# Kernel optimization log

Measured on AMD Instinct MI355X. Metric: run time of the kernel, lower is better.

Reference implementation:

```python
import jax, jax.numpy as jnp
import numpy as np

N_SITES = 100000
DIM = 128
KSIZE = 7  # 7^3 = 343 offsets
GRID = 160


def _build_sparse_structure(seed=0):
    """Sample N_SITES unique voxels in a GRID^3 volume and build the
    depthwise-conv kernel map: neighbor_idx[i, k] = index of site at
    coords[i] + offset[k], or N_SITES (sentinel -> zero row) if absent."""
    rng = np.random.default_rng(seed)
    lin = rng.choice(GRID ** 3, size=N_SITES, replace=False)
    coords = np.stack(np.unravel_index(lin, (GRID, GRID, GRID)), axis=1).astype(np.int64)  # [N,3]
    lookup = np.full(GRID ** 3, N_SITES, dtype=np.int32)
    lookup[lin] = np.arange(N_SITES, dtype=np.int32)
    r = KSIZE // 2
    offs = np.stack(np.meshgrid(*([np.arange(-r, r + 1)] * 3), indexing="ij"), axis=-1).reshape(-1, 3)  # [343,3]
    K = offs.shape[0]
    neighbor_idx = np.full((N_SITES, K), N_SITES, dtype=np.int32)
    for k in range(K):
        nb = coords + offs[k]
        ok = np.all((nb >= 0) & (nb < GRID), axis=1)
        nb_lin = (nb[ok, 0] * GRID + nb[ok, 1]) * GRID + nb[ok, 2]
        neighbor_idx[ok, k] = lookup[nb_lin]
    return neighbor_idx


def setup_inputs() -> dict:
    key = jax.random.key(0)
    ks = jax.random.split(key, 12)
    neighbor_idx = jnp.asarray(_build_sparse_structure(0))
    d, h = DIM, 4 * DIM
    K = KSIZE ** 3
    return {
        "feats": jax.random.normal(ks[0], (N_SITES, d), jnp.float32),
        "neighbor_idx": neighbor_idx,
        "dw_w": jax.random.normal(ks[1], (K, d), jnp.float32) * 0.05,
        "dw_b": jax.random.normal(ks[2], (d,), jnp.float32) * 0.02,
        "ln_g": 1.0 + 0.1 * jax.random.normal(ks[3], (d,), jnp.float32),
        "ln_b": 0.02 * jax.random.normal(ks[4], (d,), jnp.float32),
        "w1": jax.random.normal(ks[5], (d, h), jnp.float32) * (1.0 / np.sqrt(d)),
        "b1": 0.02 * jax.random.normal(ks[6], (h,), jnp.float32),
        "grn_g": 0.1 * jax.random.normal(ks[7], (1, h), jnp.float32),
        "grn_b": 0.02 * jax.random.normal(ks[8], (1, h), jnp.float32),
        "w2": jax.random.normal(ks[9], (h, d), jnp.float32) * (1.0 / np.sqrt(h)),
        "b2": 0.02 * jax.random.normal(ks[10], (d,), jnp.float32),
    }


def reference(feats, neighbor_idx, dw_w, dw_b, ln_g, ln_b, w1, b1, grn_g, grn_b, w2, b2):
    eps = 1e-6
    n, d = feats.shape
    # --- sparse depthwise conv: gather-multiply-accumulate over kernel offsets ---
    f_pad = jnp.concatenate([feats, jnp.zeros((1, d), feats.dtype)], axis=0)  # sentinel row

    def step(acc, xs):
        idx_k, w_k = xs  # idx_k: [N], w_k: [dim]
        return acc + f_pad[idx_k] * w_k, None

    x, _ = jax.lax.scan(step, jnp.zeros_like(feats), (neighbor_idx.T, dw_w))
    x = x + dw_b
    # --- LayerNorm over channels ---
    mu = jnp.mean(x, axis=-1, keepdims=True)
    var = jnp.var(x, axis=-1, keepdims=True)
    x = (x - mu) / jnp.sqrt(var + eps) * ln_g + ln_b
    # --- pwconv1 -> GELU (exact, matching torch default) ---
    x = jax.nn.gelu(x @ w1 + b1, approximate=False)  # [N, 4*dim]
    # --- GRN: L2 norm over all sites (dim=0), per channel ---
    gx = jnp.sqrt(jnp.sum(x * x, axis=0, keepdims=True))  # [1, 4*dim]
    nx = gx / (jnp.mean(gx, axis=-1, keepdims=True) + eps)
    x = grn_g * (x * nx) + grn_b + x
    # --- pwconv2 + residual (drop_path identity in eval) ---
    x = x @ w2 + b2
    return feats + x
```

## Files before the change

### kernel.cpp

```cpp
#include <hip/hip_runtime.h>

typedef unsigned short u16;
typedef unsigned int u32;
typedef __attribute__((ext_vector_type(8))) short bf16x8;
typedef __attribute__((ext_vector_type(4))) float f32x4;

__device__ __forceinline__ u16 f2bf(float f) {
    u32 u = __float_as_uint(f);
    return (u16)((u + 0x7FFFu + ((u >> 16) & 1u)) >> 16);
}

__device__ __forceinline__ float fast_gelu(float x) {
    const float t = x * x;
    const float y2 = x * __builtin_fmaf(0.0713548214f, t, 1.5957691216057308f);
    const float u = __expf(fminf(y2, 80.f));
    return x * u * __builtin_amdgcn_rcpf(u + 1.f);
}

__device__ __forceinline__ void gload_lds16(const u16* g, u16* l) {
    __builtin_amdgcn_global_load_lds(
        (const __attribute__((address_space(1))) void*)g,
        (__attribute__((address_space(3))) void*)l, 16, 0, 0);
}

__global__ __launch_bounds__(256) void dwln_k(
    const float* __restrict__ feats, const int* __restrict__ nb,
    const float* __restrict__ dw_w, const float* __restrict__ dw_b,
    const float* __restrict__ ln_g, const float* __restrict__ ln_b,
    u16* __restrict__ xln, int nsites)
{
    __shared__ int lists[4][344];
    const int w = threadIdx.x >> 6;
    const int lane = threadIdx.x & 63;
    const int s = blockIdx.x * 4 + w;
    if (s >= nsites) return;
    const int* row = nb + (size_t)s * 343;
    int idx[6];
    #pragma unroll
    for (int j = 0; j < 5; ++j) idx[j] = row[lane + j * 64];
    idx[5] = (lane < 23) ? row[320 + lane] : nsites;
    int c = 0;
    #pragma unroll
    for (int i = 0; i < 6; ++i) c += (idx[i] < nsites) ? 1 : 0;
    int pre = c;
    #pragma unroll
    for (int off = 1; off < 64; off <<= 1) {
        const int v = __shfl_up(pre, off, 64);
        if (lane >= off) pre += v;
    }
    const int cnt = __shfl(pre, 63, 64);
    pre -= c;
    int p = pre;
    #pragma unroll
    for (int i = 0; i < 6; ++i) {
        const int k = (i < 5) ? (lane + i * 64) : (320 + lane);
        if (idx[i] < nsites) lists[w][p++] = idx[i] | (k << 17);
    }
    float x0 = 0.f, x1 = 0.f;
    for (int base = 0; base < cnt; base += 8) {
        float2 f[8], wv[8];
        #pragma unroll
        for (int i = 0; i < 8; ++i) {
            if (base + i < cnt) {
                const int e = lists[w][base + i];
                f[i]  = *(const float2*)(feats + (size_t)(e & 0x1FFFF) * 128 + lane * 2);
                wv[i] = *(const float2*)(dw_w + (size_t)(e >> 17) * 128 + lane * 2);
            } else { f[i] = float2{0.f, 0.f}; wv[i] = float2{0.f, 0.f}; }
        }
        #pragma unroll
        for (int i = 0; i < 8; ++i) {
            x0 += f[i].x * wv[i].x;
            x1 += f[i].y * wv[i].y;
        }
    }
    const float2 bv = *(const float2*)(dw_b + lane * 2);
    const float2 gv = *(const float2*)(ln_g + lane * 2);
    const float2 lbv = *(const float2*)(ln_b + lane * 2);
    float a0 = x0 + bv.x, a1 = x1 + bv.y;
    float sm = a0 + a1, ss = a0 * a0 + a1 * a1;
    #pragma unroll
    for (int off = 32; off > 0; off >>= 1) {
        sm += __shfl_xor(sm, off, 64);
        ss += __shfl_xor(ss, off, 64);
    }
    const float mean = sm * (1.f / 128.f);
    const float var = ss * (1.f / 128.f) - mean * mean;
    const float rstd = rsqrtf(fmaxf(var, 0.f) + 1e-6f);
    const float y0 = (a0 - mean) * rstd * gv.x + lbv.x;
    const float y1 = (a1 - mean) * rstd * gv.y + lbv.y;
    *(u32*)(xln + (size_t)s * 128 + lane * 2) =
        (u32)f2bf(y0) | ((u32)f2bf(y1) << 16);
}

__global__ __launch_bounds__(256) void transpose_w1_k(
    const float* __restrict__ w1, u16* __restrict__ w1t)
{
    const int e = blockIdx.x * 256 + threadIdx.x;
    const int n = e >> 7, k = e & 127;
    w1t[e] = f2bf(w1[k * 512 + n]);
}

__global__ __launch_bounds__(256, 4) void gemm1_k(
    const u16* __restrict__ xln, const u16* __restrict__ w1t,
    const float* __restrict__ b1, u16* __restrict__ h,
    float* __restrict__ gx_sq, int nsites)
{
    __shared__ u16 xb[64 * 128];
    __shared__ float s_red[128];
    const int t = threadIdx.x;
    const int n0 = blockIdx.x * 128;
    const int m0 = blockIdx.y * 64;
    const int lane = t & 63;
    const int w = t >> 6;
    const int wn = w * 32;
    const int l15 = lane & 15, quad = lane >> 4;
    if (t < 128) s_red[t] = 0.f;
    #pragma unroll
    for (int i = 0; i < 4; ++i) {
        const int r = w * 16 + i * 4 + (lane >> 4);
        const int c = (lane & 15) ^ (r & 15);
        gload_lds16(xln + (size_t)(m0 + r) * 128 + c * 8,
                    &xb[(w * 16 + i * 4) * 128]);
    }
    f32x4 acc[2][4];
    #pragma unroll
    for (int i = 0; i < 2; ++i)
        #pragma unroll
        for (int j = 0; j < 4; ++j) acc[i][j] = f32x4{0.f, 0.f, 0.f, 0.f};
    const u16* a_base = w1t + (size_t)(n0 + wn + l15) * 128 + quad * 8;
    bf16x8 aC[2];
    #pragma unroll
    for (int nt = 0; nt < 2; ++nt) aC[nt] = *(const bf16x8*)(a_base + (size_t)nt * 16 * 128);
    asm volatile("s_waitcnt vmcnt(0)" ::: "memory");
    __syncthreads();
    #pragma unroll
    for (int ks = 0; ks < 4; ++ks) {
        bf16x8 aN[2];
        if (ks < 3) {
            #pragma unroll
            for (int nt = 0; nt < 2; ++nt)
                aN[nt] = *(const bf16x8*)(a_base + (size_t)nt * 16 * 128 + (ks + 1) * 32);
        }
        bf16x8 b[4];
        #pragma unroll
        for (int mt = 0; mt < 4; ++mt) {
            const int r = mt * 16 + l15;
            b[mt] = *(const bf16x8*)(&xb[r * 128 + (((ks * 4 + quad) ^ l15) << 3)]);
        }
        #pragma unroll
        for (int nt = 0; nt < 2; ++nt)
            #pragma unroll
            for (int mt = 0; mt < 4; ++mt)
                acc[nt][mt] = __builtin_amdgcn_mfma_f32_16x16x32_bf16(aC[nt], b[mt], acc[nt][mt], 0, 0, 0);
        if (ks < 3) {
            #pragma unroll
            for (int nt = 0; nt < 2; ++nt) aC[nt] = aN[nt];
        }
    }
    float ssl[2][4] = {{0.f,0.f,0.f,0.f},{0.f,0.f,0.f,0.f}};
    #pragma unroll
    for (int nt = 0; nt < 2; ++nt) {
        const int chb = n0 + wn + nt * 16 + quad * 4;
        const float4 b1v = *(const float4*)(b1 + chb);
        #pragma unroll
        for (int mt = 0; mt < 4; ++mt) {
            const int site = m0 + mt * 16 + l15;
            if (site < nsites) {
                float v[4];
                #pragma unroll
                for (int rg = 0; rg < 4; ++rg) {
                    v[rg] = fast_gelu(acc[nt][mt][rg] + ((const float*)&b1v)[rg]);
                    ssl[nt][rg] += v[rg] * v[rg];
                }
                uint2 o;
                o.x = (u32)f2bf(v[0]) | ((u32)f2bf(v[1]) << 16);
                o.y = (u32)f2bf(v[2]) | ((u32)f2bf(v[3]) << 16);
                *(uint2*)(h + (size_t)site * 512 + chb) = o;
            }
        }
    }
    #pragma unroll
    for (int nt = 0; nt < 2; ++nt)
        #pragma unroll
        for (int rg = 0; rg < 4; ++rg) {
            float v = ssl[nt][rg];
            v += __shfl_xor(v, 1, 64);
            v += __shfl_xor(v, 2, 64);
            v += __shfl_xor(v, 4, 64);
            v += __shfl_xor(v, 8, 64);
            if (l15 == 0) atomicAdd(&s_red[wn + nt * 16 + quad * 4 + rg], v);
        }
    __syncthreads();
    if (t < 128) atomicAdd(&gx_sq[n0 + t], s_red[t]);
}

__global__ __launch_bounds__(256) void beff_k(
    const float* __restrict__ grn_b, const float* __restrict__ w2,
    float* __restrict__ b_eff)
{
    __shared__ float red[256];
    const int t = threadIdx.x;
    const int dc = t & 127, part = t >> 7;
    const int c0 = blockIdx.x * 64 + part * 32;
    float p = 0.f;
    #pragma unroll 8
    for (int i = 0; i < 32; ++i) {
        const int c = c0 + i;
        p += grn_b[c] * w2[(size_t)c * 128 + dc];
    }
    red[t] = p;
    __syncthreads();
    if (t < 128) atomicAdd(&b_eff[t], red[t] + red[t + 128]);
}

__global__ __launch_bounds__(512) void grn_scale_k(
    const float* __restrict__ gx_sq, const float* __restrict__ grn_g,
    float* __restrict__ scale)
{
    __shared__ float red[512];
    const int t = threadIdx.x;
    const float g = sqrtf(gx_sq[t]);
    red[t] = g;
    __syncthreads();
    #pragma unroll
    for (int off = 256; off > 0; off >>= 1) {
        if (t < off) red[t] += red[t + off];
        __syncthreads();
    }
    const float mean = red[0] * (1.f / 512.f);
    scale[t] = grn_g[t] * (g / (mean + 1e-6f)) + 1.f;
}

__global__ __launch_bounds__(256) void w2t_k(
    const float* __restrict__ scale, const float* __restrict__ w2,
    u16* __restrict__ w2t)
{
    const int e = blockIdx.x * 256 + threadIdx.x;
    const int c = e & 511, dc = e >> 9;
    w2t[e] = f2bf(scale[c] * w2[(size_t)c * 128 + dc]);
}

__global__ __launch_bounds__(256, 4) void gemm2_k(
    const u16* __restrict__ h, const u16* __restrict__ w2t,
    const float* __restrict__ b_eff, const float* __restrict__ b2,
    const float* __restrict__ feats,
    float* __restrict__ out, int nsites)
{
    __shared__ u16 hb[2][64 * 128];
    const int t = threadIdx.x;
    const int m0 = blockIdx.x * 64;
    const int lane = t & 63;
    const int w = t >> 6;
    const int wn = w * 32;
    const int l15 = lane & 15, quad = lane >> 4;
    f32x4 acc[2][4];
    #pragma unroll
    for (int i = 0; i < 2; ++i)
        #pragma unroll
        for (int j = 0; j < 2 * 2; ++j) acc[i & 1][j] = f32x4{0.f, 0.f, 0.f, 0.f};
    #pragma unroll
    for (int i = 0; i < 2; ++i)
        #pragma unroll
        for (int j = 0; j < 4; ++j) acc[i][j] = f32x4{0.f, 0.f, 0.f, 0.f};
    const u16* a_base = w2t + (size_t)(wn + l15) * 512 + quad * 8;

    #define STAGE2(bsel, tc)                                                     \
        {                                                                        \
            _Pragma("unroll")                                                    \
            for (int i_ = 0; i_ < 4; ++i_) {                                     \
                const int r_ = w * 16 + i_ * 4 + (lane >> 4);                    \
                const int c_ = (lane & 15) ^ (r_ & 15);                          \
                gload_lds16(h + (size_t)(m0 + r_) * 512 + (tc) * 128 + c_ * 8,   \
                            &hb[bsel][(w * 16 + i_ * 4) * 128]);                 \
            }                                                                    \
        }

    STAGE2(0, 0)
    bf16x8 aC[2];
    #pragma unroll
    for (int nt = 0; nt < 2; ++nt) aC[nt] = *(const bf16x8*)(a_base + (size_t)nt * 16 * 512);
    asm volatile("s_waitcnt vmcnt(0)" ::: "memory");
    __syncthreads();
    #pragma unroll
    for (int tch = 0; tch < 4; ++tch) {
        const int cur = tch & 1;
        if (tch < 3) STAGE2(cur ^ 1, tch + 1)
        #pragma unroll
        for (int ks = 0; ks < 4; ++ks) {
            const int ksg = tch * 4 + ks;
            bf16x8 aN[2];
            if (ksg < 15) {
                #pragma unroll
                for (int nt = 0; nt < 2; ++nt)
                    aN[nt] = *(const bf16x8*)(a_base + (size_t)nt * 16 * 512 + (ksg + 1) * 32);
            }
            bf16x8 b[4];
            #pragma unroll
            for (int mt = 0; mt < 4; ++mt) {
                const int r = mt * 16 + l15;
                b[mt] = *(const bf16x8*)(&hb[cur][r * 128 + (((ks * 4 + quad) ^ l15) << 3)]);
            }
            #pragma unroll
            for (int nt = 0; nt < 2; ++nt)
                #pragma unroll
                for (int mt = 0; mt < 4; ++mt)
                    acc[nt][mt] = __builtin_amdgcn_mfma_f32_16x16x32_bf16(aC[nt], b[mt], acc[nt][mt], 0, 0, 0);
            if (ksg < 15) {
                #pragma unroll
                for (int nt = 0; nt < 2; ++nt) aC[nt] = aN[nt];
            }
        }
        if (tch < 3) {
            asm volatile("s_waitcnt vmcnt(0)" ::: "memory");
            __syncthreads();
        }
    }
    #undef STAGE2
    #pragma unroll
    for (int nt = 0; nt < 2; ++nt) {
        const int chb = wn + nt * 16 + quad * 4;
        const float4 bev = *(const float4*)(b_eff + chb);
        const float4 b2v = *(const float4*)(b2 + chb);
        #pragma unroll
        for (int mt = 0; mt < 4; ++mt) {
            const int site = m0 + mt * 16 + l15;
            if (site < nsites) {
                const float4 fv = *(const float4*)(feats + (size_t)site * 128 + chb);
                float4 o;
                o.x = acc[nt][mt][0] + bev.x + b2v.x + fv.x;
                o.y = acc[nt][mt][1] + bev.y + b2v.y + fv.y;
                o.z = acc[nt][mt][2] + bev.z + b2v.z + fv.z;
                o.w = acc[nt][mt][3] + bev.w + b2v.w + fv.w;
                *(float4*)(out + (size_t)site * 128 + chb) = o;
            }
        }
    }
}

extern "C" void kernel_launch(void* const* d_in, const int* in_sizes, int n_in,
                              void* d_out, int out_size, void* d_ws, size_t ws_size,
                              hipStream_t stream) {
    const float* feats = (const float*)d_in[0];
    const int* nb      = (const int*)d_in[1];
    const float* dw_w  = (const float*)d_in[2];
    const float* dw_b  = (const float*)d_in[3];
    const float* ln_g  = (const float*)d_in[4];
    const float* ln_b  = (const float*)d_in[5];
    const float* w1    = (const float*)d_in[6];
    const float* b1    = (const float*)d_in[7];
    const float* grn_g = (const float*)d_in[8];
    const float* grn_b = (const float*)d_in[9];
    const float* w2    = (const float*)d_in[10];
    const float* b2    = (const float*)d_in[11];
    float* out = (float*)d_out;
    const int nsites = in_sizes[0] / 128;

    char* ws = (char*)d_ws;
    size_t off = 0;
    u16* xln   = (u16*)(ws + off);  off += (((size_t)(nsites + 128) * 128 * 2) + 255) & ~(size_t)255;
    u16* h     = (u16*)(ws + off);  off += (((size_t)(nsites + 128) * 512 * 2) + 255) & ~(size_t)255;
    u16* w1t   = (u16*)(ws + off);  off += 512 * 128 * 2;
    u16* w2t   = (u16*)(ws + off);  off += 128 * 512 * 2;
    float* gx_sq = (float*)(ws + off); off += 512 * 4;
    float* scale = (float*)(ws + off); off += 512 * 4;
    float* b_eff = (float*)(ws + off); off += 128 * 4;

    hipMemsetAsync(gx_sq, 0, 512 * sizeof(float), stream);
    hipMemsetAsync(b_eff, 0, 128 * sizeof(float), stream);
    transpose_w1_k<<<256, 256, 0, stream>>>(w1, w1t);
    beff_k<<<8, 256, 0, stream>>>(grn_b, w2, b_eff);
    dwln_k<<<(nsites + 3) / 4, 256, 0, stream>>>(feats, nb, dw_w, dw_b, ln_g, ln_b, xln, nsites);
    const int m1blocks = (nsites + 63) / 64;
    gemm1_k<<<dim3(4, m1blocks), 256, 0, stream>>>(xln, w1t, b1, h, gx_sq, nsites);
    grn_scale_k<<<1, 512, 0, stream>>>(gx_sq, grn_g, scale);
    w2t_k<<<256, 256, 0, stream>>>(scale, w2, w2t);
    const int m2blocks = (nsites + 63) / 64;
    gemm2_k<<<m2blocks, 256, 0, stream>>>(h, w2t, b_eff, b2, feats, out, nsites);
}
```

Measured before the change: 427.8 us.

## Gather bf16 copies of feats and dw weights in sparse depthwise conv

Adds a cast kernel that converts feats and dw_w to bf16 ahead of time, with a zeroed sentinel row, so the depthwise gather reads half the bytes per neighbor. The neighbor list compaction now uses ballot/popcount instead of a shuffle-based prefix scan. The list is padded to a multiple of 8 with sentinel entries, which removes the per-element bounds branch in the gather loop. Costs are an extra pass over feats and lower precision in the conv accumulation inputs.

```diff
diff --git a/kernel.cpp b/kernel.cpp
--- a/kernel.cpp
+++ b/kernel.cpp
@@ -23,13 +23,25 @@
         (__attribute__((address_space(3))) void*)l, 16, 0, 0);
 }
 
+__global__ __launch_bounds__(256) void cast_feats_k(
+    const float* __restrict__ src, u16* __restrict__ dst, int n4)
+{
+    const int e = blockIdx.x * 256 + threadIdx.x;
+    if (e >= n4) return;
+    const float4 v = *(const float4*)(src + (size_t)e * 4);
+    uint2 o;
+    o.x = (u32)f2bf(v.x) | ((u32)f2bf(v.y) << 16);
+    o.y = (u32)f2bf(v.z) | ((u32)f2bf(v.w) << 16);
+    *(uint2*)(dst + (size_t)e * 4) = o;
+}
+
 __global__ __launch_bounds__(256) void dwln_k(
-    const float* __restrict__ feats, const int* __restrict__ nb,
-    const float* __restrict__ dw_w, const float* __restrict__ dw_b,
+    const u16* __restrict__ featsb, const int* __restrict__ nb,
+    const u16* __restrict__ dwwb, const float* __restrict__ dw_b,
     const float* __restrict__ ln_g, const float* __restrict__ ln_b,
     u16* __restrict__ xln, int nsites)
 {
-    __shared__ int lists[4][344];
+    __shared__ int lists[4][352];
     const int w = threadIdx.x >> 6;
     const int lane = threadIdx.x & 63;
     const int s = blockIdx.x * 4 + w;
@@ -39,38 +51,32 @@
     #pragma unroll
     for (int j = 0; j < 5; ++j) idx[j] = row[lane + j * 64];
     idx[5] = (lane < 23) ? row[320 + lane] : nsites;
-    int c = 0;
-    #pragma unroll
-    for (int i = 0; i < 6; ++i) c += (idx[i] < nsites) ? 1 : 0;
-    int pre = c;
-    #pragma unroll
-    for (int off = 1; off < 64; off <<= 1) {
-        const int v = __shfl_up(pre, off, 64);
-        if (lane >= off) pre += v;
-    }
-    const int cnt = __shfl(pre, 63, 64);
-    pre -= c;
-    int p = pre;
+    const unsigned long long below = ((1ull << lane) - 1ull);
+    int cnt = 0;
     #pragma unroll
     for (int i = 0; i < 6; ++i) {
+        const bool v = idx[i] < nsites;
+        const unsigned long long bal = __ballot(v);
         const int k = (i < 5) ? (lane + i * 64) : (320 + lane);
-        if (idx[i] < nsites) lists[w][p++] = idx[i] | (k << 17);
-    }
+        if (v) lists[w][cnt + __popcll(bal & below)] = idx[i] | (k << 17);
+        cnt += (int)__popcll(bal);
+    }
+    const int cntp = (cnt + 7) & ~7;
+    if (lane < cntp - cnt) lists[w][cnt + lane] = nsites;
+    __builtin_amdgcn_s_waitcnt(0);
     float x0 = 0.f, x1 = 0.f;
-    for (int base = 0; base < cnt; base += 8) {
-        float2 f[8], wv[8];
+    for (int base = 0; base < cntp; base += 8) {
+        u32 f[8], wv[8];
         #pragma unroll
         for (int i = 0; i < 8; ++i) {
-            if (base + i < cnt) {
-                const int e = lists[w][base + i];
-                f[i]  = *(const float2*)(feats + (size_t)(e & 0x1FFFF) * 128 + lane * 2);
-                wv[i] = *(const float2*)(dw_w + (size_t)(e >> 17) * 128 + lane * 2);
-            } else { f[i] = float2{0.f, 0.f}; wv[i] = float2{0.f, 0.f}; }
+            const int e = lists[w][base + i];
+            f[i]  = *(const u32*)(featsb + (size_t)(e & 0x1FFFF) * 128 + lane * 2);
+            wv[i] = *(const u32*)(dwwb + (size_t)(e >> 17) * 128 + lane * 2);
         }
         #pragma unroll
         for (int i = 0; i < 8; ++i) {
-            x0 += f[i].x * wv[i].x;
-            x1 += f[i].y * wv[i].y;
+            x0 += __uint_as_float(f[i] << 16) * __uint_as_float(wv[i] << 16);
+            x1 += __uint_as_float(f[i] & 0xFFFF0000u) * __uint_as_float(wv[i] & 0xFFFF0000u);
         }
     }
     const float2 bv = *(const float2*)(dw_b + lane * 2);
@@ -254,10 +260,6 @@
     const int wn = w * 32;
     const int l15 = lane & 15, quad = lane >> 4;
     f32x4 acc[2][4];
-    #pragma unroll
-    for (int i = 0; i < 2; ++i)
-        #pragma unroll
-        for (int j = 0; j < 2 * 2; ++j) acc[i & 1][j] = f32x4{0.f, 0.f, 0.f, 0.f};
     #pragma unroll
     for (int i = 0; i < 2; ++i)
         #pragma unroll
@@ -359,6 +361,8 @@
     size_t off = 0;
     u16* xln   = (u16*)(ws + off);  off += (((size_t)(nsites + 128) * 128 * 2) + 255) & ~(size_t)255;
     u16* h     = (u16*)(ws + off);  off += (((size_t)(nsites + 128) * 512 * 2) + 255) & ~(size_t)255;
+    u16* featsb= (u16*)(ws + off);  off += (((size_t)(nsites + 1) * 128 * 2) + 255) & ~(size_t)255;
+    u16* dwwb  = (u16*)(ws + off);  off += 343 * 128 * 2 + 128;
     u16* w1t   = (u16*)(ws + off);  off += 512 * 128 * 2;
     u16* w2t   = (u16*)(ws + off);  off += 128 * 512 * 2;
     float* gx_sq = (float*)(ws + off); off += 512 * 4;
@@ -367,9 +371,14 @@
 
     hipMemsetAsync(gx_sq, 0, 512 * sizeof(float), stream);
     hipMemsetAsync(b_eff, 0, 128 * sizeof(float), stream);
+    hipMemsetAsync(featsb + (size_t)nsites * 128, 0, 128 * sizeof(u16), stream);
+    const int nfeat4 = nsites * 32;
+    cast_feats_k<<<(nfeat4 + 255) / 256, 256, 0, stream>>>(feats, featsb, nfeat4);
+    const int ndww4 = 343 * 32;
+    cast_feats_k<<<(ndww4 + 255) / 256, 256, 0, stream>>>(dw_w, dwwb, ndww4);
     transpose_w1_k<<<256, 256, 0, stream>>>(w1, w1t);
     beff_k<<<8, 256, 0, stream>>>(grn_b, w2, b_eff);
-    dwln_k<<<(nsites + 3) / 4, 256, 0, stream>>>(feats, nb, dw_w, dw_b, ln_g, ln_b, xln, nsites);
+    dwln_k<<<(nsites + 3) / 4, 256, 0, stream>>>(featsb, nb, dwwb, dw_b, ln_g, ln_b, xln, nsites);
     const int m1blocks = (nsites + 63) / 64;
     gemm1_k<<<dim3(4, m1blocks), 256, 0, stream>>>(xln, w1t, b1, h, gx_sq, nsites);
     grn_scale_k<<<1, 512, 0, stream>>>(gx_sq, grn_g, scale);
```

Result: faster. 413.0 us (-3.5%).
